# Performance work log

Measured on AMD Instinct MI355X. Metric: run time of the kernel, lower is better.

The kernel has to match this reference:

```python
import jax, jax.numpy as jnp
import numpy as np

NHEADS = 8
HEAD_DIM = 64  # odim // nheads = 512 // 8


def setup_inputs() -> dict:
    key = jax.random.key(0)
    ks = jax.random.split(key, 5)
    B, S, D = 2, 4096, 512
    scale = 1.0 / np.sqrt(D)
    return {
        "m_feats": jax.random.normal(ks[0], (B, S, D), dtype=jnp.float32),
        "Wc": jax.random.normal(ks[1], (2 * D, D), dtype=jnp.float32) * scale,
        "bc": jax.random.normal(ks[2], (2 * D,), dtype=jnp.float32) * 0.01,
        "Wv": jax.random.normal(ks[3], (D, D), dtype=jnp.float32) * scale,
        "bv": jax.random.normal(ks[4], (D,), dtype=jnp.float32) * 0.01,
    }


def reference(m_feats, Wc, bc, Wv, bv):
    # eval mode: dropout(p=0.5) is identity
    B, S, D = m_feats.shape
    H, Dh = NHEADS, HEAD_DIM
    m_k = m_feats @ Wv.T + bv                    # [B,S,D]
    m_trans = m_feats @ Wc.T + bc                # [B,S,2D]
    m_q, m_v = m_trans[..., :D], m_trans[..., D:]
    # torch.split into contiguous per-head chunks == reshape to [B,S,H,Dh]
    k = m_k.reshape(B, S, H, Dh)
    q = m_q.reshape(B, S, H, Dh)
    v = m_v.reshape(B, S, H, Dh)
    # scores[b,h,i,j] = k_i . q_j / sqrt(Dh); softmax over j (the q axis)
    scores = jnp.einsum("bihd,bjhd->bhij", k, q) / np.sqrt(Dh).astype(np.float32)
    w = jax.nn.softmax(scores, axis=-1)          # [B,H,S,S]
    r = jnp.einsum("bhij,bjhd->bihd", w, v).reshape(B, S, D)
    return m_feats + r
```

## Files before the change

### kernel.cpp

```cpp
#include <hip/hip_runtime.h>

#define MTOT 8192

typedef __attribute__((ext_vector_type(8))) short bf16x8;
typedef __attribute__((ext_vector_type(4))) float f32x4;

#if __has_builtin(__builtin_amdgcn_exp2f)
#define EXP2F __builtin_amdgcn_exp2f
#else
#define EXP2F exp2f
#endif

#define SC 0.18033688011112042f
#define LDP 72
#define CTS 136

static __device__ __forceinline__ unsigned short tb(float f) {
  union { float f; unsigned int i; } x;
  x.f = f;
  return (unsigned short)(x.i >> 16);
}
static __device__ __forceinline__ unsigned int pkt(float a, float b) {
  union { float f; unsigned int i; } xa, xb;
  xa.f = a; xb.f = b;
  return (xa.i >> 16) | (xb.i & 0xFFFF0000u);
}
static __device__ __forceinline__ bf16x8 ld8f32_bf16(const float* __restrict__ p) {
  f32x4 lo = *(const f32x4*)p;
  f32x4 hi = *(const f32x4*)(p + 4);
  union { unsigned int u[4]; bf16x8 v; } r;
  r.u[0] = pkt(lo[0], lo[1]);
  r.u[1] = pkt(lo[2], lo[3]);
  r.u[2] = pkt(hi[0], hi[1]);
  r.u[3] = pkt(hi[2], hi[3]);
  return r.v;
}

__global__ __launch_bounds__(256) void gemm_qvk(
    const float* __restrict__ mf,
    const float* __restrict__ Wc,
    const float* __restrict__ bc,
    const float* __restrict__ Wv,
    const float* __restrict__ bv,
    unsigned short* __restrict__ ws,
    int nct)
{
  const int bid = blockIdx.x;
  const int tn = bid % nct, tm = bid / nct;
  const int w = threadIdx.x >> 6, lane = threadIdx.x & 63;
  const int n = lane & 15, q = lane >> 4;

  __shared__ alignas(16) unsigned short smem[2 * 128 * LDP];
  unsigned short* As = smem;
  unsigned short* Bs = smem + 128 * LDP;

  f32x4 acc[4][4] = {};
  const int rowA0 = tm * 128, colB0 = tn * 128;
  const int sr = threadIdx.x >> 4;
  const int sc = (threadIdx.x & 15) * 4;

  for (int kc = 0; kc < 512; kc += 64) {
    __syncthreads();
#pragma unroll
    for (int rr = 0; rr < 8; ++rr) {
      const int row = rr * 16 + sr;
      f32x4 av = *(const f32x4*)(mf + (size_t)(rowA0 + row) * 512 + kc + sc);
      uint2 ap; ap.x = pkt(av[0], av[1]); ap.y = pkt(av[2], av[3]);
      *(uint2*)(&As[row * LDP + sc]) = ap;
      const int c = colB0 + row;
      const float* bsrc = (c < 1024) ? (Wc + (size_t)c * 512)
                                     : (Wv + (size_t)(c - 1024) * 512);
      f32x4 bvx = *(const f32x4*)(bsrc + kc + sc);
      uint2 bp; bp.x = pkt(bvx[0], bvx[1]); bp.y = pkt(bvx[2], bvx[3]);
      *(uint2*)(&Bs[row * LDP + sc]) = bp;
    }
    __syncthreads();
#pragma unroll
    for (int ks = 0; ks < 2; ++ks) {
      bf16x8 a[4], b[4];
#pragma unroll
      for (int si = 0; si < 4; ++si)
        a[si] = *(const bf16x8*)(&As[((w >> 1) * 64 + si * 16 + n) * LDP + ks * 32 + q * 8]);
#pragma unroll
      for (int sj = 0; sj < 4; ++sj)
        b[sj] = *(const bf16x8*)(&Bs[((w & 1) * 64 + sj * 16 + n) * LDP + ks * 32 + q * 8]);
#pragma unroll
      for (int si = 0; si < 4; ++si)
#pragma unroll
        for (int sj = 0; sj < 4; ++sj)
          acc[si][sj] = __builtin_amdgcn_mfma_f32_16x16x32_bf16(a[si], b[sj], acc[si][sj], 0, 0, 0);
    }
  }

  __syncthreads();
  unsigned short* Ct = smem;
  const bool isV = (tn >= 4 && tn < 8);
  const int rl0 = (w >> 1) * 64, cl0 = (w & 1) * 64;

  if (!isV) {
    const bool isK = (tn >= 8);
#pragma unroll
    for (int sj = 0; sj < 4; ++sj) {
      const int c = colB0 + sj * 16 + n;
      const float bias = isK ? bv[c - 1024] : bc[c];
#pragma unroll
      for (int si = 0; si < 4; ++si)
#pragma unroll
        for (int r = 0; r < 4; ++r) {
          float v = acc[si][sj][r] + bias;
          if (isK) v *= SC;
          Ct[(rl0 + si * 16 + q * 4 + r) * CTS + cl0 + sj * 16 + n] = tb(v);
        }
    }
  } else {
#pragma unroll
    for (int sj = 0; sj < 4; ++sj) {
      const float bias = bc[colB0 + sj * 16 + n];
#pragma unroll
      for (int si = 0; si < 4; ++si) {
        uint2 pk;
        pk.x = pkt(acc[si][sj][0] + bias, acc[si][sj][1] + bias);
        pk.y = pkt(acc[si][sj][2] + bias, acc[si][sj][3] + bias);
        *(uint2*)(&Ct[(cl0 + sj * 16 + n) * CTS + rl0 + si * 16 + q * 4]) = pk;
      }
    }
  }
  __syncthreads();

  const int rk = threadIdx.x & 7, rr2 = threadIdx.x >> 3;
#pragma unroll
  for (int rp = 0; rp < 4; ++rp) {
    const int row = rp * 32 + rr2;
#pragma unroll
    for (int ch = 0; ch < 2; ++ch) {
      const int col = ch * 64 + rk * 8;
      bf16x8 v = *(const bf16x8*)(&Ct[row * CTS + col]);
      if (!isV) {
        const int srow = rowA0 + row;
        const int bb = srow >> 12, ss = srow & 4095;
        const int cg = colB0 + col;
        const int cl = (cg >= 1024) ? (cg - 1024) : cg;
        const int hh = cl >> 6, dh0 = cl & 63;
        unsigned short* base = (cg >= 1024) ? (ws + (size_t)2 * MTOT * 512) : ws;
        *(bf16x8*)(base + ((size_t)((bb * 8 + hh) * 4096 + ss)) * 64 + dh0) = v;
      } else {
        const int cv = (tn - 4) * 128 + row;
        const int hh = cv >> 6, dh0 = cv & 63;
        const int sg = rowA0 + col;
        const int bb = sg >> 12, ss = sg & 4095;
        *(bf16x8*)(ws + (size_t)MTOT * 512 +
                   ((size_t)((bb * 8 + hh) * 64 + dh0)) * 4096 + ss) = v;
      }
    }
  }
}

template <bool KWS>
__global__ __launch_bounds__(128, 2) void attn_kernel(
    const unsigned short* __restrict__ qvws,
    const float* __restrict__ mf,
    const float* __restrict__ Wv,
    const float* __restrict__ bv,
    float* __restrict__ out)
{
  const int bid = blockIdx.x;
  const int bh = ((bid & 7) << 1) | ((bid >> 3) & 1);
  const int ib = bid >> 4;
  const int b_ = bh >> 3, h = bh & 7;
  const int w = threadIdx.x >> 6, lane = threadIdx.x & 63;
  const int n = lane & 15, q = lane >> 4;
  const int i0 = ib * 64;

  __shared__ alignas(16) unsigned short PK[2][64 * LDP];
  __shared__ float lbuf[64];

  const unsigned short* Qb = qvws + (size_t)(bh * 4096) * 64;
  const unsigned short* Vb = qvws + (size_t)MTOT * 512 + (size_t)(bh * 64) * 4096;

  bf16x8 aK[4][2];
  if (KWS) {
    const unsigned short* Kb = qvws + (size_t)2 * MTOT * 512 + (size_t)(bh * 4096) * 64;
#pragma unroll
    for (int sub = 0; sub < 4; ++sub)
#pragma unroll
      for (int s = 0; s < 2; ++s)
        aK[sub][s] = *(const bf16x8*)(Kb + (size_t)(i0 + sub * 16 + n) * 64 + s * 32 + q * 8);
  } else {
    f32x4 ka[2][4] = {};
    for (int kk = 0; kk < 512; kk += 32) {
      bf16x8 a0 = ld8f32_bf16(mf + (size_t)(b_ * 4096 + i0 + (2 * w + 0) * 16 + n) * 512 + kk + q * 8);
      bf16x8 a1 = ld8f32_bf16(mf + (size_t)(b_ * 4096 + i0 + (2 * w + 1) * 16 + n) * 512 + kk + q * 8);
#pragma unroll
      for (int t = 0; t < 4; ++t) {
        bf16x8 bw = ld8f32_bf16(Wv + (size_t)(h * 64 + t * 16 + n) * 512 + kk + q * 8);
        ka[0][t] = __builtin_amdgcn_mfma_f32_16x16x32_bf16(a0, bw, ka[0][t], 0, 0, 0);
        ka[1][t] = __builtin_amdgcn_mfma_f32_16x16x32_bf16(a1, bw, ka[1][t], 0, 0, 0);
      }
    }
#pragma unroll
    for (int sl = 0; sl < 2; ++sl)
#pragma unroll
      for (int t = 0; t < 4; ++t) {
        const float bias = bv[h * 64 + t * 16 + n];
#pragma unroll
        for (int r = 0; r < 4; ++r)
          PK[0][((2 * w + sl) * 16 + q * 4 + r) * LDP + t * 16 + n] =
              tb((ka[sl][t][r] + bias) * SC);
      }
    __syncthreads();
#pragma unroll
    for (int sub = 0; sub < 4; ++sub)
#pragma unroll
      for (int s = 0; s < 2; ++s)
        aK[sub][s] = *(const bf16x8*)(&PK[0][(sub * 16 + n) * LDP + s * 32 + q * 8]);
    __syncthreads();
  }

  f32x4 o[4][4] = {};
  f32x4 lacc[4] = {};
  const bf16x8 ones = {(short)0x3F80, (short)0x3F80, (short)0x3F80, (short)0x3F80,
                       (short)0x3F80, (short)0x3F80, (short)0x3F80, (short)0x3F80};
  unsigned short* Pw = &PK[w][0];
  const int jbase = w * 2048;

  bf16x8 bq[4][2], bvv[4][2];
#pragma unroll
  for (int jt = 0; jt < 4; ++jt)
#pragma unroll
    for (int s = 0; s < 2; ++s)
      bq[jt][s] = *(const bf16x8*)(Qb + (size_t)(jbase + jt * 16 + n) * 64 + s * 32 + q * 8);
#pragma unroll
  for (int t = 0; t < 4; ++t)
#pragma unroll
    for (int s = 0; s < 2; ++s)
      bvv[t][s] = *(const bf16x8*)(Vb + (size_t)(t * 16 + n) * 4096 + jbase + s * 32 + q * 8);

  for (int it = 0; it < 32; ++it) {
    const int j1 = jbase + ((it + 1) & 31) * 64;

#pragma unroll
    for (int sub = 0; sub < 4; ++sub) {
      f32x4 c[4] = {};
#pragma unroll
      for (int jt = 0; jt < 4; ++jt)
#pragma unroll
        for (int s = 0; s < 2; ++s)
          c[jt] = __builtin_amdgcn_mfma_f32_16x16x32_bf16(bq[jt][s], aK[sub][s], c[jt], 0, 0, 0);
#pragma unroll
      for (int jt = 0; jt < 4; ++jt) {
        uint2 pk;
        pk.x = pkt(EXP2F(c[jt][0]), EXP2F(c[jt][1]));
        pk.y = pkt(EXP2F(c[jt][2]), EXP2F(c[jt][3]));
        *(uint2*)(Pw + (sub * 16 + n) * LDP + jt * 16 + q * 4) = pk;
      }
    }

#pragma unroll
    for (int jt = 0; jt < 4; ++jt)
#pragma unroll
      for (int s = 0; s < 2; ++s)
        bq[jt][s] = *(const bf16x8*)(Qb + (size_t)(j1 + jt * 16 + n) * 64 + s * 32 + q * 8);

    asm volatile("s_waitcnt lgkmcnt(0)" ::: "memory");

#pragma unroll
    for (int s = 0; s < 2; ++s) {
#pragma unroll
      for (int sub = 0; sub < 4; ++sub) {
        bf16x8 pa = *(const bf16x8*)(Pw + (sub * 16 + n) * LDP + s * 32 + q * 8);
        lacc[sub] = __builtin_amdgcn_mfma_f32_16x16x32_bf16(pa, ones, lacc[sub], 0, 0, 0);
#pragma unroll
        for (int t = 0; t < 4; ++t)
          o[sub][t] = __builtin_amdgcn_mfma_f32_16x16x32_bf16(pa, bvv[t][s], o[sub][t], 0, 0, 0);
      }
    }

#pragma unroll
    for (int t = 0; t < 4; ++t)
#pragma unroll
      for (int s = 0; s < 2; ++s)
        bvv[t][s] = *(const bf16x8*)(Vb + (size_t)(t * 16 + n) * 4096 + j1 + s * 32 + q * 8);
  }

  __syncthreads();
  float* mO = (float*)&PK[0][0];
  const int ebase = (w == 0) ? 0 : 32;
  const int rbase = (w == 0) ? 32 : 0;
  const int esub0 = (w == 0) ? 2 : 0;
  const int ksub0 = (w == 0) ? 0 : 2;
#pragma unroll
  for (int sl = 0; sl < 2; ++sl) {
    const int sub = esub0 + sl;
#pragma unroll
    for (int t = 0; t < 4; ++t)
#pragma unroll
      for (int r = 0; r < 4; ++r)
        mO[(ebase + sl * 16 + q * 4 + r) * 68 + t * 16 + n] = o[sub][t][r];
    if (n == 0)
#pragma unroll
      for (int r = 0; r < 4; ++r)
        lbuf[ebase + sl * 16 + q * 4 + r] = lacc[sub][r];
  }
  __syncthreads();
#pragma unroll
  for (int sl = 0; sl < 2; ++sl) {
    const int sub = ksub0 + sl;
    float li[4];
#pragma unroll
    for (int r = 0; r < 4; ++r)
      li[r] = 1.0f / (lacc[sub][r] + lbuf[rbase + sl * 16 + q * 4 + r]);
#pragma unroll
    for (int t = 0; t < 4; ++t) {
#pragma unroll
      for (int r = 0; r < 4; ++r) {
        const int i = i0 + sub * 16 + q * 4 + r;
        const int dh = t * 16 + n;
        const size_t idx = (size_t)(b_ * 4096 + i) * 512 + h * 64 + dh;
        out[idx] = (o[sub][t][r] + mO[(rbase + sl * 16 + q * 4 + r) * 68 + t * 16 + n]) * li[r]
                   + mf[idx];
      }
    }
  }
}

extern "C" void kernel_launch(void* const* d_in, const int* in_sizes, int n_in,
                              void* d_out, int out_size, void* d_ws, size_t ws_size,
                              hipStream_t stream) {
  const float* mf = (const float*)d_in[0];
  const float* Wc = (const float*)d_in[1];
  const float* bc = (const float*)d_in[2];
  const float* Wv = (const float*)d_in[3];
  const float* bv = (const float*)d_in[4];
  float* out = (float*)d_out;
  unsigned short* ws = (unsigned short*)d_ws;

  const bool kws = ws_size >= (size_t)3 * MTOT * 512 * 2;
  const int nct = kws ? 12 : 8;

  gemm_qvk<<<64 * nct, 256, 0, stream>>>(mf, Wc, bc, Wv, bv, ws, nct);
  if (kws)
    attn_kernel<true><<<1024, 128, 0, stream>>>(ws, mf, Wv, bv, out);
  else
    attn_kernel<false><<<1024, 128, 0, stream>>>(ws, mf, Wv, bv, out);
}
```

Baseline: 250.8 us.

## Halve attention row tile, double grid, compute row sums with VALU shuffles

The query-row tile per block in the attention kernel shrinks from 64 to 32 and the grid doubles to 2048 blocks. The j-step drops to 32 columns and launch bounds rise to allow 4 blocks per CU. The softmax denominator is now accumulated with scalar adds and cross-lane shuffles instead of an extra MFMA against a ones vector. V is loaded at the top of each iteration rather than prefetched for the next one. The aim is higher occupancy and fewer matrix ops, at the cost of reloading Q and V twice as often overall and exposing V load latency.

```diff
diff --git a/kernel.cpp b/kernel.cpp
--- a/kernel.cpp
+++ b/kernel.cpp
@@ -14,6 +14,7 @@
 #define SC 0.18033688011112042f
 #define LDP 72
 #define CTS 136
+#define PST 40
 
 static __device__ __forceinline__ unsigned short tb(float f) {
   union { float f; unsigned int i; } x;
@@ -156,7 +157,7 @@
 }
 
 template <bool KWS>
-__global__ __launch_bounds__(128, 2) void attn_kernel(
+__global__ __launch_bounds__(128, 4) void attn_kernel(
     const unsigned short* __restrict__ qvws,
     const float* __restrict__ mf,
     const float* __restrict__ Wv,
@@ -169,94 +170,92 @@
   const int b_ = bh >> 3, h = bh & 7;
   const int w = threadIdx.x >> 6, lane = threadIdx.x & 63;
   const int n = lane & 15, q = lane >> 4;
-  const int i0 = ib * 64;
-
-  __shared__ alignas(16) unsigned short PK[2][64 * LDP];
-  __shared__ float lbuf[64];
+  const int i0 = ib * 32;
+
+  __shared__ alignas(16) unsigned short PK[2][32 * PST];
+  __shared__ alignas(16) float mO[32 * 68];
+  __shared__ float lbuf[2][32];
 
   const unsigned short* Qb = qvws + (size_t)(bh * 4096) * 64;
   const unsigned short* Vb = qvws + (size_t)MTOT * 512 + (size_t)(bh * 64) * 4096;
 
-  bf16x8 aK[4][2];
+  bf16x8 aK[2][2];
   if (KWS) {
     const unsigned short* Kb = qvws + (size_t)2 * MTOT * 512 + (size_t)(bh * 4096) * 64;
 #pragma unroll
-    for (int sub = 0; sub < 4; ++sub)
+    for (int sub = 0; sub < 2; ++sub)
 #pragma unroll
       for (int s = 0; s < 2; ++s)
         aK[sub][s] = *(const bf16x8*)(Kb + (size_t)(i0 + sub * 16 + n) * 64 + s * 32 + q * 8);
   } else {
-    f32x4 ka[2][4] = {};
+    f32x4 ka[4] = {};
     for (int kk = 0; kk < 512; kk += 32) {
-      bf16x8 a0 = ld8f32_bf16(mf + (size_t)(b_ * 4096 + i0 + (2 * w + 0) * 16 + n) * 512 + kk + q * 8);
-      bf16x8 a1 = ld8f32_bf16(mf + (size_t)(b_ * 4096 + i0 + (2 * w + 1) * 16 + n) * 512 + kk + q * 8);
+      bf16x8 a0 = ld8f32_bf16(mf + (size_t)(b_ * 4096 + i0 + w * 16 + n) * 512 + kk + q * 8);
 #pragma unroll
       for (int t = 0; t < 4; ++t) {
         bf16x8 bw = ld8f32_bf16(Wv + (size_t)(h * 64 + t * 16 + n) * 512 + kk + q * 8);
-        ka[0][t] = __builtin_amdgcn_mfma_f32_16x16x32_bf16(a0, bw, ka[0][t], 0, 0, 0);
-        ka[1][t] = __builtin_amdgcn_mfma_f32_16x16x32_bf16(a1, bw, ka[1][t], 0, 0, 0);
+        ka[t] = __builtin_amdgcn_mfma_f32_16x16x32_bf16(a0, bw, ka[t], 0, 0, 0);
       }
     }
-#pragma unroll
-    for (int sl = 0; sl < 2; ++sl)
-#pragma unroll
-      for (int t = 0; t < 4; ++t) {
-        const float bias = bv[h * 64 + t * 16 + n];
-#pragma unroll
-        for (int r = 0; r < 4; ++r)
-          PK[0][((2 * w + sl) * 16 + q * 4 + r) * LDP + t * 16 + n] =
-              tb((ka[sl][t][r] + bias) * SC);
-      }
+    unsigned short* Kt = &PK[0][0];
+#pragma unroll
+    for (int t = 0; t < 4; ++t) {
+      const float bias = bv[h * 64 + t * 16 + n];
+#pragma unroll
+      for (int r = 0; r < 4; ++r)
+        Kt[(w * 16 + q * 4 + r) * LDP + t * 16 + n] = tb((ka[t][r] + bias) * SC);
+    }
     __syncthreads();
 #pragma unroll
-    for (int sub = 0; sub < 4; ++sub)
+    for (int sub = 0; sub < 2; ++sub)
 #pragma unroll
       for (int s = 0; s < 2; ++s)
-        aK[sub][s] = *(const bf16x8*)(&PK[0][(sub * 16 + n) * LDP + s * 32 + q * 8]);
+        aK[sub][s] = *(const bf16x8*)(&Kt[(sub * 16 + n) * LDP + s * 32 + q * 8]);
     __syncthreads();
   }
 
-  f32x4 o[4][4] = {};
-  f32x4 lacc[4] = {};
-  const bf16x8 ones = {(short)0x3F80, (short)0x3F80, (short)0x3F80, (short)0x3F80,
-                       (short)0x3F80, (short)0x3F80, (short)0x3F80, (short)0x3F80};
+  f32x4 o[2][4] = {};
+  float lsc[2] = {0.0f, 0.0f};
   unsigned short* Pw = &PK[w][0];
   const int jbase = w * 2048;
 
-  bf16x8 bq[4][2], bvv[4][2];
-#pragma unroll
-  for (int jt = 0; jt < 4; ++jt)
+  bf16x8 bq[2][2], bvv[4];
+#pragma unroll
+  for (int jt = 0; jt < 2; ++jt)
 #pragma unroll
     for (int s = 0; s < 2; ++s)
       bq[jt][s] = *(const bf16x8*)(Qb + (size_t)(jbase + jt * 16 + n) * 64 + s * 32 + q * 8);
-#pragma unroll
-  for (int t = 0; t < 4; ++t)
-#pragma unroll
-    for (int s = 0; s < 2; ++s)
-      bvv[t][s] = *(const bf16x8*)(Vb + (size_t)(t * 16 + n) * 4096 + jbase + s * 32 + q * 8);
-
-  for (int it = 0; it < 32; ++it) {
-    const int j1 = jbase + ((it + 1) & 31) * 64;
-
-#pragma unroll
-    for (int sub = 0; sub < 4; ++sub) {
-      f32x4 c[4] = {};
-#pragma unroll
-      for (int jt = 0; jt < 4; ++jt)
+
+  for (int it = 0; it < 64; ++it) {
+    const int jc = jbase + it * 32;
+    const int j1 = jbase + ((it + 1) & 63) * 32;
+
+#pragma unroll
+    for (int t = 0; t < 4; ++t)
+      bvv[t] = *(const bf16x8*)(Vb + (size_t)(t * 16 + n) * 4096 + jc + q * 8);
+
+#pragma unroll
+    for (int sub = 0; sub < 2; ++sub) {
+      f32x4 c[2] = {};
+#pragma unroll
+      for (int jt = 0; jt < 2; ++jt)
 #pragma unroll
         for (int s = 0; s < 2; ++s)
           c[jt] = __builtin_amdgcn_mfma_f32_16x16x32_bf16(bq[jt][s], aK[sub][s], c[jt], 0, 0, 0);
 #pragma unroll
-      for (int jt = 0; jt < 4; ++jt) {
+      for (int jt = 0; jt < 2; ++jt) {
+        float e0 = EXP2F(c[jt][0]), e1 = EXP2F(c[jt][1]);
+        float e2 = EXP2F(c[jt][2]), e3 = EXP2F(c[jt][3]);
+        lsc[sub] += (e0 + e1) + (e2 + e3);
         uint2 pk;
-        pk.x = pkt(EXP2F(c[jt][0]), EXP2F(c[jt][1]));
-        pk.y = pkt(EXP2F(c[jt][2]), EXP2F(c[jt][3]));
-        *(uint2*)(Pw + (sub * 16 + n) * LDP + jt * 16 + q * 4) = pk;
+        pk.x = pkt(e0, e1);
+        pk.y = pkt(e2, e3);
+        *(uint2*)(Pw + (sub * 16 + n) * PST + jt * 16 + q * 4) = pk;
       }
     }
 
 #pragma unroll
-    for (int jt = 0; jt < 4; ++jt)
+    for (int jt = 0; jt < 2; ++jt)
 #pragma unroll
       for (int s = 0; s < 2; ++s)
         bq[jt][s] = *(const bf16x8*)(Qb + (size_t)(j1 + jt * 16 + n) * 64 + s * 32 + q * 8);
@@ -264,61 +263,49 @@
     asm volatile("s_waitcnt lgkmcnt(0)" ::: "memory");
 
 #pragma unroll
-    for (int s = 0; s < 2; ++s) {
-#pragma unroll
-      for (int sub = 0; sub < 4; ++sub) {
-        bf16x8 pa = *(const bf16x8*)(Pw + (sub * 16 + n) * LDP + s * 32 + q * 8);
-        lacc[sub] = __builtin_amdgcn_mfma_f32_16x16x32_bf16(pa, ones, lacc[sub], 0, 0, 0);
-#pragma unroll
-        for (int t = 0; t < 4; ++t)
-          o[sub][t] = __builtin_amdgcn_mfma_f32_16x16x32_bf16(pa, bvv[t][s], o[sub][t], 0, 0, 0);
-      }
-    }
-
-#pragma unroll
-    for (int t = 0; t < 4; ++t)
-#pragma unroll
-      for (int s = 0; s < 2; ++s)
-        bvv[t][s] = *(const bf16x8*)(Vb + (size_t)(t * 16 + n) * 4096 + j1 + s * 32 + q * 8);
-  }
-
+    for (int sub = 0; sub < 2; ++sub) {
+      bf16x8 pa = *(const bf16x8*)(Pw + (sub * 16 + n) * PST + q * 8);
+#pragma unroll
+      for (int t = 0; t < 4; ++t)
+        o[sub][t] = __builtin_amdgcn_mfma_f32_16x16x32_bf16(pa, bvv[t], o[sub][t], 0, 0, 0);
+    }
+  }
+
+  float lw[2];
+#pragma unroll
+  for (int sub = 0; sub < 2; ++sub) {
+    float v = lsc[sub];
+    v += __shfl_xor(v, 16, 64);
+    v += __shfl_xor(v, 32, 64);
+    lw[sub] = v;
+  }
+  const int esub = 1 - w, ksub = w;
+#pragma unroll
+  for (int t = 0; t < 4; ++t)
+#pragma unroll
+    for (int r = 0; r < 4; ++r)
+      mO[(esub * 16 + q * 4 + r) * 68 + t * 16 + n] = o[esub][t][r];
+  if (lane < 16) {
+    lbuf[w][lane] = lw[0];
+    lbuf[w][16 + lane] = lw[1];
+  }
   __syncthreads();
-  float* mO = (float*)&PK[0][0];
-  const int ebase = (w == 0) ? 0 : 32;
-  const int rbase = (w == 0) ? 32 : 0;
-  const int esub0 = (w == 0) ? 2 : 0;
-  const int ksub0 = (w == 0) ? 0 : 2;
-#pragma unroll
-  for (int sl = 0; sl < 2; ++sl) {
-    const int sub = esub0 + sl;
-#pragma unroll
-    for (int t = 0; t < 4; ++t)
-#pragma unroll
-      for (int r = 0; r < 4; ++r)
-        mO[(ebase + sl * 16 + q * 4 + r) * 68 + t * 16 + n] = o[sub][t][r];
-    if (n == 0)
-#pragma unroll
-      for (int r = 0; r < 4; ++r)
-        lbuf[ebase + sl * 16 + q * 4 + r] = lacc[sub][r];
-  }
-  __syncthreads();
-#pragma unroll
-  for (int sl = 0; sl < 2; ++sl) {
-    const int sub = ksub0 + sl;
-    float li[4];
-#pragma unroll
-    for (int r = 0; r < 4; ++r)
-      li[r] = 1.0f / (lacc[sub][r] + lbuf[rbase + sl * 16 + q * 4 + r]);
-#pragma unroll
-    for (int t = 0; t < 4; ++t) {
-#pragma unroll
-      for (int r = 0; r < 4; ++r) {
-        const int i = i0 + sub * 16 + q * 4 + r;
-        const int dh = t * 16 + n;
-        const size_t idx = (size_t)(b_ * 4096 + i) * 512 + h * 64 + dh;
-        out[idx] = (o[sub][t][r] + mO[(rbase + sl * 16 + q * 4 + r) * 68 + t * 16 + n]) * li[r]
-                   + mf[idx];
-      }
+
+  float li[4];
+#pragma unroll
+  for (int r = 0; r < 4; ++r) {
+    const int il = ksub * 16 + q * 4 + r;
+    li[r] = 1.0f / (lbuf[0][il] + lbuf[1][il]);
+  }
+#pragma unroll
+  for (int t = 0; t < 4; ++t) {
+#pragma unroll
+    for (int r = 0; r < 4; ++r) {
+      const int i = i0 + ksub * 16 + q * 4 + r;
+      const int dh = t * 16 + n;
+      const size_t idx = (size_t)(b_ * 4096 + i) * 512 + h * 64 + dh;
+      out[idx] = (o[ksub][t][r] + mO[(ksub * 16 + q * 4 + r) * 68 + t * 16 + n]) * li[r]
+                 + mf[idx];
     }
   }
 }
@@ -339,7 +326,7 @@
 
   gemm_qvk<<<64 * nct, 256, 0, stream>>>(mf, Wc, bc, Wv, bv, ws, nct);
   if (kws)
-    attn_kernel<true><<<1024, 128, 0, stream>>>(ws, mf, Wv, bv, out);
+    attn_kernel<true><<<2048, 128, 0, stream>>>(ws, mf, Wv, bv, out);
   else
-    attn_kernel<false><<<1024, 128, 0, stream>>>(ws, mf, Wv, bv, out);
-}
+    attn_kernel<false><<<2048, 128, 0, stream>>>(ws, mf, Wv, bv, out);
+}
```

Measured after the change: 343.8 us. 37.0% more time.

## Software-pipeline QK MFMAs per sub-tile and compute row sums with scalar adds

Applied to the files above, without the earlier changes.

Restructures the inner loop so the QK^T MFMAs for the next sub-tile are issued before the exp/pack/PV work of the current one, interleaving the LDS round-trip and PV MFMAs per sub-tile instead of in one batch. The Q prefetch moves earlier inside the loop. The softmax denominator is now accumulated in fp32 from the unrounded exponentials, with cross-lane shuffles at the end, instead of an extra MFMA against a ones vector. This removes 8 MFMAs per iteration and should overlap the exp latency with the matrix cores, at the cost of more live registers (c[4][4]), more VALU adds, and more lgkmcnt waits.

```diff
diff --git a/kernel.cpp b/kernel.cpp
--- a/kernel.cpp
+++ b/kernel.cpp
@@ -172,7 +172,7 @@
   const int i0 = ib * 64;
 
   __shared__ alignas(16) unsigned short PK[2][64 * LDP];
-  __shared__ float lbuf[64];
+  __shared__ float lbuf[2][64];
 
   const unsigned short* Qb = qvws + (size_t)(bh * 4096) * 64;
   const unsigned short* Vb = qvws + (size_t)MTOT * 512 + (size_t)(bh * 64) * 4096;
@@ -217,9 +217,7 @@
   }
 
   f32x4 o[4][4] = {};
-  f32x4 lacc[4] = {};
-  const bf16x8 ones = {(short)0x3F80, (short)0x3F80, (short)0x3F80, (short)0x3F80,
-                       (short)0x3F80, (short)0x3F80, (short)0x3F80, (short)0x3F80};
+  float lsc[4] = {0.0f, 0.0f, 0.0f, 0.0f};
   unsigned short* Pw = &PK[w][0];
   const int jbase = w * 2048;
 
@@ -238,37 +236,50 @@
   for (int it = 0; it < 32; ++it) {
     const int j1 = jbase + ((it + 1) & 31) * 64;
 
+    f32x4 c[4][4];
+#pragma unroll
+    for (int jt = 0; jt < 4; ++jt) {
+      f32x4 z = {};
+      z = __builtin_amdgcn_mfma_f32_16x16x32_bf16(bq[jt][0], aK[0][0], z, 0, 0, 0);
+      z = __builtin_amdgcn_mfma_f32_16x16x32_bf16(bq[jt][1], aK[0][1], z, 0, 0, 0);
+      c[0][jt] = z;
+    }
+
 #pragma unroll
     for (int sub = 0; sub < 4; ++sub) {
-      f32x4 c[4] = {};
-#pragma unroll
-      for (int jt = 0; jt < 4; ++jt)
-#pragma unroll
-        for (int s = 0; s < 2; ++s)
-          c[jt] = __builtin_amdgcn_mfma_f32_16x16x32_bf16(bq[jt][s], aK[sub][s], c[jt], 0, 0, 0);
+      if (sub < 3) {
+#pragma unroll
+        for (int jt = 0; jt < 4; ++jt) {
+          f32x4 z = {};
+          z = __builtin_amdgcn_mfma_f32_16x16x32_bf16(bq[jt][0], aK[sub + 1][0], z, 0, 0, 0);
+          z = __builtin_amdgcn_mfma_f32_16x16x32_bf16(bq[jt][1], aK[sub + 1][1], z, 0, 0, 0);
+          c[sub + 1][jt] = z;
+        }
+      }
+      if (sub == 2) {
+#pragma unroll
+        for (int jt = 0; jt < 4; ++jt)
+#pragma unroll
+          for (int s = 0; s < 2; ++s)
+            bq[jt][s] = *(const bf16x8*)(Qb + (size_t)(j1 + jt * 16 + n) * 64 + s * 32 + q * 8);
+      }
+
 #pragma unroll
       for (int jt = 0; jt < 4; ++jt) {
+        float e0 = EXP2F(c[sub][jt][0]), e1 = EXP2F(c[sub][jt][1]);
+        float e2 = EXP2F(c[sub][jt][2]), e3 = EXP2F(c[sub][jt][3]);
+        lsc[sub] += (e0 + e1) + (e2 + e3);
         uint2 pk;
-        pk.x = pkt(EXP2F(c[jt][0]), EXP2F(c[jt][1]));
-        pk.y = pkt(EXP2F(c[jt][2]), EXP2F(c[jt][3]));
+        pk.x = pkt(e0, e1);
+        pk.y = pkt(e2, e3);
         *(uint2*)(Pw + (sub * 16 + n) * LDP + jt * 16 + q * 4) = pk;
       }
-    }
-
-#pragma unroll
-    for (int jt = 0; jt < 4; ++jt)
-#pragma unroll
-      for (int s = 0; s < 2; ++s)
-        bq[jt][s] = *(const bf16x8*)(Qb + (size_t)(j1 + jt * 16 + n) * 64 + s * 32 + q * 8);
-
-    asm volatile("s_waitcnt lgkmcnt(0)" ::: "memory");
-
-#pragma unroll
-    for (int s = 0; s < 2; ++s) {
-#pragma unroll
-      for (int sub = 0; sub < 4; ++sub) {
+
+      asm volatile("s_waitcnt lgkmcnt(0)" ::: "memory");
+
+#pragma unroll
+      for (int s = 0; s < 2; ++s) {
         bf16x8 pa = *(const bf16x8*)(Pw + (sub * 16 + n) * LDP + s * 32 + q * 8);
-        lacc[sub] = __builtin_amdgcn_mfma_f32_16x16x32_bf16(pa, ones, lacc[sub], 0, 0, 0);
 #pragma unroll
         for (int t = 0; t < 4; ++t)
           o[sub][t] = __builtin_amdgcn_mfma_f32_16x16x32_bf16(pa, bvv[t][s], o[sub][t], 0, 0, 0);
@@ -280,6 +291,15 @@
 #pragma unroll
       for (int s = 0; s < 2; ++s)
         bvv[t][s] = *(const bf16x8*)(Vb + (size_t)(t * 16 + n) * 4096 + j1 + s * 32 + q * 8);
+  }
+
+  float lw[4];
+#pragma unroll
+  for (int sub = 0; sub < 4; ++sub) {
+    float v = lsc[sub];
+    v += __shfl_xor(v, 16, 64);
+    v += __shfl_xor(v, 32, 64);
+    lw[sub] = v;
   }
 
   __syncthreads();
@@ -296,10 +316,11 @@
 #pragma unroll
       for (int r = 0; r < 4; ++r)
         mO[(ebase + sl * 16 + q * 4 + r) * 68 + t * 16 + n] = o[sub][t][r];
-    if (n == 0)
-#pragma unroll
-      for (int r = 0; r < 4; ++r)
-        lbuf[ebase + sl * 16 + q * 4 + r] = lacc[sub][r];
+  }
+  if (lane < 16) {
+#pragma unroll
+    for (int sub = 0; sub < 4; ++sub)
+      lbuf[w][sub * 16 + lane] = lw[sub];
   }
   __syncthreads();
 #pragma unroll
@@ -307,8 +328,10 @@
     const int sub = ksub0 + sl;
     float li[4];
 #pragma unroll
-    for (int r = 0; r < 4; ++r)
-      li[r] = 1.0f / (lacc[sub][r] + lbuf[rbase + sl * 16 + q * 4 + r]);
+    for (int r = 0; r < 4; ++r) {
+      const int il = sub * 16 + q * 4 + r;
+      li[r] = 1.0f / (lbuf[0][il] + lbuf[1][il]);
+    }
 #pragma unroll
     for (int t = 0; t < 4; ++t) {
 #pragma unroll
```

Result: faster. 239.6 us (-4.5%).
